# Optimization experiments

Measured on AMD Instinct MI355X. Metric: run time of the kernel, lower is better.

Reference implementation:

```python
import jax, jax.numpy as jnp
import numpy as np

KP_EXTENT = 1.2  # influence radius of each kernel point (init arg KP_extent)
SHADOW_COORD = 1e6  # shadow point coordinate for padding (as in original KPConv)


def setup_inputs() -> dict:
    key = jax.random.key(0)
    k1, k2, k3, k4, k5, k6 = jax.random.split(key, 6)
    N, Ns, H, K, Cin, Cout = 20000, 20000, 40, 15, 128, 128
    q_pts = jax.random.uniform(k1, (N, 3), dtype=jnp.float32)
    s_pts = jax.random.uniform(k2, (Ns, 3), dtype=jnp.float32)
    neighb_inds = jax.random.randint(k3, (N, H), 0, Ns, dtype=jnp.int32)
    x = jax.random.normal(k4, (Ns, Cin), dtype=jnp.float32)
    # kernel point positions inside the sphere (stand-in for load_kernels output)
    kernel_points = jax.random.normal(k5, (K, 3), dtype=jnp.float32) * 0.5
    kernel_points = kernel_points.at[0].set(0.0)  # fixed='center'
    weights = jax.random.normal(k6, (K, Cin, Cout), dtype=jnp.float32) * (1.0 / np.sqrt(Cin))
    return {"q_pts": q_pts, "s_pts": s_pts, "neighb_inds": neighb_inds,
            "x": x, "kernel_points": kernel_points, "weights": weights}


def reference(q_pts, s_pts, neighb_inds, x, kernel_points, weights):
    # Pad support points with a far-away shadow point and features with a zero row,
    # so out-of-range neighbor index Ns contributes nothing (original KPConv trick).
    s_pad = jnp.concatenate([s_pts, jnp.full((1, s_pts.shape[1]), SHADOW_COORD, s_pts.dtype)], axis=0)
    x_pad = jnp.concatenate([x, jnp.zeros((1, x.shape[1]), x.dtype)], axis=0)

    # Gather neighbor coords, center on query points: [N, H, 3]
    neighbors = s_pad[neighb_inds] - q_pts[:, None, :]

    # Squared distance to every kernel point: [N, H, K]
    diff = neighbors[:, :, None, :] - kernel_points[None, None, :, :]
    sq_dist = jnp.sum(diff * diff, axis=-1)

    # Linear influence weights, aggregation_mode='sum': [N, K, H]
    all_weights = jnp.clip(1.0 - jnp.sqrt(sq_dist) / KP_EXTENT, 0.0, None)
    all_weights = jnp.swapaxes(all_weights, 1, 2)

    # Gather neighbor features: [N, H, Cin]
    neighb_x = x_pad[neighb_inds]

    # Influence-weighted aggregation over neighbors: [N, K, Cin]
    weighted = jnp.einsum('nkh,nhc->nkc', all_weights, neighb_x)

    # Per-kernel-point linear maps, summed over kernel points: [N, Cout]
    out = jnp.einsum('nkc,kcd->nd', weighted, weights)
    return out
```

## Files before the change

### kernel.cpp

```cpp
#include <hip/hip_runtime.h>

#define KP   15
#define HN   40
#define CIN  128
#define COUT 128
#define KDIM (KP*CIN)
#define KP_EXT_INV (1.0f/1.2f)
#define GBM  32
#define GBK  128

typedef __bf16 bf16x8 __attribute__((ext_vector_type(8)));
typedef __bf16 bf16x4 __attribute__((ext_vector_type(4)));
typedef float  f32x4  __attribute__((ext_vector_type(4)));

__device__ inline void async_copy16(const void* g, void* lds) {
    __builtin_amdgcn_global_load_lds(
        (const __attribute__((address_space(1))) unsigned int*)g,
        (__attribute__((address_space(3))) unsigned int*)lds, 16, 0, 0);
}
#define LGKM0() __asm__ __volatile__("s_waitcnt lgkmcnt(0)" ::: "memory")
#define VM0()   __asm__ __volatile__("s_waitcnt vmcnt(0)"   ::: "memory")

__global__ __launch_bounds__(256)
void kpconv_prep(const float* __restrict__ x, const float* __restrict__ W,
                 __bf16* __restrict__ xb, __bf16* __restrict__ Wt,
                 int nx_elems, int nxB)
{
    __shared__ float sW[32][133];
    const int b = blockIdx.x;
    const int t = threadIdx.x;

    if (b < nxB) {
        const int e0 = (b*256 + t) * 8;
        if (e0 + 8 <= nx_elems) {
            const float4 f0 = *(const float4*)(x + e0);
            const float4 f1 = *(const float4*)(x + e0 + 4);
            bf16x8 v;
            v[0]=(__bf16)f0.x; v[1]=(__bf16)f0.y; v[2]=(__bf16)f0.z; v[3]=(__bf16)f0.w;
            v[4]=(__bf16)f1.x; v[5]=(__bf16)f1.y; v[6]=(__bf16)f1.z; v[7]=(__bf16)f1.w;
            *(bf16x8*)(xb + e0) = v;
        } else {
            for (int e = e0; e < nx_elems; ++e) xb[e] = (__bf16)x[e];
        }
    } else {
        const int kc0 = (b - nxB) * 32;
        #pragma unroll
        for (int i = 0; i < 4; ++i) {
            const int off = t*4 + i*1024;
            const int r = off >> 7, c = off & 127;
            const float4 f = *(const float4*)(W + (size_t)(kc0 + r)*COUT + c);
            sW[r][c+0]=f.x; sW[r][c+1]=f.y; sW[r][c+2]=f.z; sW[r][c+3]=f.w;
        }
        __syncthreads();
        #pragma unroll
        for (int i = 0; i < 2; ++i) {
            const int id = t + i*256;
            const int d  = id >> 2, ch = id & 3;
            bf16x8 v;
            #pragma unroll
            for (int j = 0; j < 8; ++j) v[j] = (__bf16)sW[ch*8 + j][d];
            *(bf16x8*)(Wt + (size_t)d*KDIM + kc0 + ch*8) = v;
        }
    }
}

union SharedU {
    struct { __bf16 sXt[4][4][128][8];
             float4 s_nd[4][HN]; int s_idx[4][HN]; } a;
    struct { __bf16 sA[GBM*GBK]; __bf16 sB[COUT*GBK]; } b;
};

__global__ __launch_bounds__(256, 3)
void kpconv_main(const float* __restrict__ q_pts,
                 const float* __restrict__ s_pts,
                 const int*   __restrict__ nb,
                 const __bf16* __restrict__ xb,
                 const float* __restrict__ kpts,
                 const __bf16* __restrict__ Wt,
                 __bf16* __restrict__ wsA,
                 float* __restrict__ out, int N, int Ns)
{
    __shared__ SharedU sh;

    const int t  = threadIdx.x;
    const int wv = t >> 6;
    const int l  = t & 63;
    const int m  = l & 15;
    const int q  = l >> 4;
    const int m0 = blockIdx.x * GBM;

    {
        float kx=0.f, ky=0.f, kz=0.f;
        if (m < KP) { kx = kpts[m*3+0]; ky = kpts[m*3+1]; kz = kpts[m*3+2]; }
        const float kk  = kx*kx + ky*ky + kz*kz;
        const float kx2 = -2.f*kx, ky2 = -2.f*ky, kz2 = -2.f*kz;

        for (int pi = 0; pi < 8; ++pi) {
            const int n = m0 + wv*8 + pi;

            if (l < HN) {
                int idx = nb[n*HN + l];
                float dx, dy, dz;
                if (idx >= 0 && idx < Ns) {
                    dx = s_pts[idx*3+0] - q_pts[n*3+0];
                    dy = s_pts[idx*3+1] - q_pts[n*3+1];
                    dz = s_pts[idx*3+2] - q_pts[n*3+2];
                } else { idx = 0; dx = dy = dz = 2.0e6f; }
                sh.a.s_idx[wv][l] = idx;
                sh.a.s_nd[wv][l]  = make_float4(dx, dy, dz, dx*dx+dy*dy+dz*dz);
            }
            LGKM0();

            uint4 g[5][2];
            #pragma unroll
            for (int it = 0; it < 5; ++it) {
                const int h0 = (it < 4) ? (it*8 + 2*q) : (32 + 2*q);
                g[it][0] = *(const uint4*)(xb + (size_t)sh.a.s_idx[wv][h0  ]*CIN + m*8);
                g[it][1] = *(const uint4*)(xb + (size_t)sh.a.s_idx[wv][h0+1]*CIN + m*8);
            }

            bf16x8 wfrag[2];
            #pragma unroll
            for (int ks = 0; ks < 2; ++ks) {
                #pragma unroll
                for (int j = 0; j < 8; ++j) {
                    const int h = ks*32 + q*8 + j;
                    float w = 0.f;
                    if (m < KP && h < HN) {
                        const float4 nd = sh.a.s_nd[wv][h];
                        const float d2 = fmaf(nd.x, kx2,
                                         fmaf(nd.y, ky2,
                                         fmaf(nd.z, kz2, nd.w + kk)));
                        const float d = __builtin_amdgcn_sqrtf(d2);
                        w = fmaxf(fmaf(d, -KP_EXT_INV, 1.0f), 0.f);
                    }
                    wfrag[ks][j] = (__bf16)w;
                }
            }

            f32x4 acc[8];
            #pragma unroll
            for (int nt = 0; nt < 8; ++nt) acc[nt] = (f32x4){0.f,0.f,0.f,0.f};

            #pragma unroll
            for (int ks = 0; ks < 2; ++ks) {
                const int itBeg = ks ? 4 : 0;
                const int itEnd = ks ? 5 : 4;
                #pragma unroll
                for (int it = itBeg; it < itEnd; ++it) {
                    const unsigned av[4] = {g[it][0].x, g[it][0].y, g[it][0].z, g[it][0].w};
                    const unsigned bv[4] = {g[it][1].x, g[it][1].y, g[it][1].z, g[it][1].w};
                    const int hc = ks ? 0 : it;
                    unsigned* plane = (unsigned*)&sh.a.sXt[wv][hc][0][0];
                    #pragma unroll
                    for (int j = 0; j < 8; ++j) {
                        const unsigned v = __builtin_amdgcn_perm(
                            bv[j>>1], av[j>>1], (j&1) ? 0x07060302u : 0x05040100u);
                        const int p = m*8 + (j ^ (m & 7));
                        plane[p*4 + q] = v;
                    }
                }
                LGKM0();
                #pragma unroll
                for (int nt = 0; nt < 8; ++nt) {
                    const int cc = nt*16 + m;
                    const int p  = (cc & ~7) | ((cc & 7) ^ ((cc >> 3) & 7));
                    bf16x8 xf = *(const bf16x8*)&sh.a.sXt[wv][q][p][0];
                    acc[nt] = __builtin_amdgcn_mfma_f32_16x16x32_bf16(
                                  xf, wfrag[ks], acc[nt], 0, 0, 0);
                }
            }

            if (m < KP) {
                #pragma unroll
                for (int nt = 0; nt < 8; ++nt) {
                    bf16x4 v;
                    #pragma unroll
                    for (int r = 0; r < 4; ++r) v[r] = (__bf16)acc[nt][r];
                    *(bf16x4*)(wsA + (size_t)n*KDIM + m*CIN + nt*16 + q*4) = v;
                }
            }
        }
    }

    VM0();
    __syncthreads();

    {
        const int rA = t >> 4;
        const int pA = t & 15;

        f32x4 acc[2][2];
        #pragma unroll
        for (int i = 0; i < 2; ++i)
            #pragma unroll
            for (int j = 0; j < 2; ++j) acc[i][j] = (f32x4){0.f,0.f,0.f,0.f};

        for (int k0 = 0; k0 < KDIM; k0 += GBK) {
            #pragma unroll
            for (int pass = 0; pass < 2; ++pass) {
                const int r  = rA + pass*16;
                const int ch = pA ^ (r & 15);
                async_copy16(wsA + (size_t)(m0 + r)*KDIM + k0 + ch*8,
                             (char*)sh.b.sA + pass*4096 + wv*1024 + l*16);
            }
            #pragma unroll
            for (int pass = 0; pass < 8; ++pass) {
                const int r  = rA + pass*16;
                const int ch = pA ^ (r & 15);
                async_copy16(Wt + (size_t)r*KDIM + k0 + ch*8,
                             (char*)sh.b.sB + pass*4096 + wv*1024 + l*16);
            }
            __syncthreads();

            #pragma unroll
            for (int ks = 0; ks < 4; ++ks) {
                bf16x8 af[2], bfr[2];
                #pragma unroll
                for (int mt = 0; mt < 2; ++mt) {
                    const int row = mt*16 + m;
                    const int p   = (ks*4 + q) ^ (row & 15);
                    af[mt] = *(const bf16x8*)&sh.b.sA[row*GBK + p*8];
                }
                #pragma unroll
                for (int j = 0; j < 2; ++j) {
                    const int row = (wv*2 + j)*16 + m;
                    const int p   = (ks*4 + q) ^ (row & 15);
                    bfr[j] = *(const bf16x8*)&sh.b.sB[row*GBK + p*8];
                }
                #pragma unroll
                for (int mt = 0; mt < 2; ++mt)
                    #pragma unroll
                    for (int j = 0; j < 2; ++j)
                        acc[mt][j] = __builtin_amdgcn_mfma_f32_16x16x32_bf16(
                                         af[mt], bfr[j], acc[mt][j], 0, 0, 0);
            }
            __syncthreads();
        }

        #pragma unroll
        for (int mt = 0; mt < 2; ++mt)
            #pragma unroll
            for (int j = 0; j < 2; ++j)
                #pragma unroll
                for (int r = 0; r < 4; ++r)
                    out[(size_t)(m0 + mt*16 + q*4 + r)*COUT
                        + (wv*2+j)*16 + m] = acc[mt][j][r];
    }
}

#define TM 8
#define WSTR (KP*CIN + 4)

__global__ __launch_bounds__(256, 2)
void kpconv_fused(const float* __restrict__ q_pts,
                  const float* __restrict__ s_pts,
                  const int*   __restrict__ nb,
                  const float* __restrict__ x,
                  const float* __restrict__ kpts,
                  const float* __restrict__ W,
                  float* __restrict__ out,
                  int N, int Ns)
{
    __shared__ float s_kp[KP*3];
    __shared__ float s_nd2[HN*3];
    __shared__ int   s_idx2[HN];
    __shared__ float s_w[KP][HN];
    __shared__ float s_wt[TM*WSTR];

    const int t  = threadIdx.x;
    const int n0 = (int)blockIdx.x * TM;
    if (t < KP*3) s_kp[t] = kpts[t];
    const int c = t & (CIN-1);
    const int g = t >> 7;

    for (int mm = 0; mm < TM; ++mm) {
        const int n = n0 + mm;
        if (t < HN) {
            float dx = 1e6f, dy = 1e6f, dz = 1e6f;
            int idx = 0;
            if (n < N) {
                idx = nb[n*HN + t];
                if (idx >= 0 && idx < Ns) {
                    dx = s_pts[idx*3+0] - q_pts[n*3+0];
                    dy = s_pts[idx*3+1] - q_pts[n*3+1];
                    dz = s_pts[idx*3+2] - q_pts[n*3+2];
                } else idx = 0;
            }
            s_idx2[t] = idx;
            s_nd2[t*3+0] = dx; s_nd2[t*3+1] = dy; s_nd2[t*3+2] = dz;
        }
        __syncthreads();
        for (int task = t; task < KP*HN; task += 256) {
            const int k = task / HN;
            const int h = task - k*HN;
            const float dx = s_nd2[h*3+0] - s_kp[k*3+0];
            const float dy = s_nd2[h*3+1] - s_kp[k*3+1];
            const float dz = s_nd2[h*3+2] - s_kp[k*3+2];
            s_w[k][h] = fmaxf(1.0f - sqrtf(dx*dx+dy*dy+dz*dz)*KP_EXT_INV, 0.0f);
        }
        __syncthreads();
        float facc[8];
        #pragma unroll
        for (int j = 0; j < 8; ++j) facc[j] = 0.0f;
        #pragma unroll 8
        for (int h = 0; h < HN; ++h) {
            const float xv = x[s_idx2[h]*CIN + c];
            #pragma unroll
            for (int j = 0; j < 8; ++j) {
                const int k = g + 2*j;
                if (k < KP) facc[j] += s_w[k][h] * xv;
            }
        }
        #pragma unroll
        for (int j = 0; j < 8; ++j) {
            const int k = g + 2*j;
            if (k < KP) s_wt[mm*WSTR + k*CIN + c] = facc[j];
        }
        __syncthreads();
    }

    const int m3 = t >> 5;
    const int d0 = (t & 31) * 4;
    const float* wm = &s_wt[m3*WSTR];
    float ax = 0.f, ay = 0.f, az = 0.f, aw = 0.f;
    #pragma unroll 4
    for (int kc = 0; kc < KP*CIN; ++kc) {
        const float  wvv = wm[kc];
        const float4 wr = *(const float4*)&W[kc*COUT + d0];
        ax += wvv * wr.x; ay += wvv * wr.y; az += wvv * wr.z; aw += wvv * wr.w;
    }
    const int n = n0 + m3;
    if (n < N) {
        float4 o; o.x = ax; o.y = ay; o.z = az; o.w = aw;
        *(float4*)&out[n*COUT + d0] = o;
    }
}

extern "C" void kernel_launch(void* const* d_in, const int* in_sizes, int n_in,
                              void* d_out, int out_size, void* d_ws, size_t ws_size,
                              hipStream_t stream) {
    const float* q_pts = (const float*)d_in[0];
    const float* s_pts = (const float*)d_in[1];
    const int*   nb    = (const int*)  d_in[2];
    const float* x     = (const float*)d_in[3];
    const float* kpts  = (const float*)d_in[4];
    const float* W     = (const float*)d_in[5];
    float* out = (float*)d_out;

    const int N  = in_sizes[0] / 3;
    const int Ns = in_sizes[1] / 3;
    const int nx = in_sizes[3];

    const size_t needA = (size_t)N * KDIM * sizeof(__bf16);
    const size_t needB = (size_t)COUT * KDIM * sizeof(__bf16);
    const size_t needX = (size_t)nx * sizeof(__bf16);

    if (ws_size >= needA + needB + needX && (N % GBM) == 0 && (nx % 8) == 0
        && (KDIM % GBK) == 0) {
        __bf16* wsA = (__bf16*)d_ws;
        __bf16* wsB = (__bf16*)((char*)d_ws + needA);
        __bf16* wsX = (__bf16*)((char*)d_ws + needA + needB);

        const int nxB = (nx/8 + 255) / 256;
        const int nwB = KDIM / 32;
        hipLaunchKernelGGL(kpconv_prep, dim3(nxB + nwB), dim3(256), 0, stream,
                           x, W, wsX, wsB, nx, nxB);
        hipLaunchKernelGGL(kpconv_main, dim3(N/GBM), dim3(256), 0, stream,
                           q_pts, s_pts, nb, wsX, kpts, wsB, wsA, out, N, Ns);
    } else {
        const int grid = (N + TM - 1) / TM;
        hipLaunchKernelGGL(kpconv_fused, dim3(grid), dim3(256), 0, stream,
                           q_pts, s_pts, nb, x, kpts, W, out, N, Ns);
    }
}
```

Before: 144.4 us.

## Keep per-point weighted features in LDS instead of global workspace round-trip

The main kernel now handles 16 points per 512-thread block, with each wave handling 2 points. It writes the bf16 [K*Cin] aggregated features into a swizzled LDS tile instead of a global workspace buffer. The second GEMM stage reads A fragments from LDS and streams B (the transposed weights) directly from global/L2 with two accumulators, dropping the async LDS staging of B. This removes roughly 77MB of workspace write and read traffic. In exchange, every block re-reads the full 128x1920 weight matrix from cache, the LDS footprint is larger, and there are fewer points per block.

```diff
diff --git a/kernel.cpp b/kernel.cpp
--- a/kernel.cpp
+++ b/kernel.cpp
@@ -5,21 +5,15 @@
 #define CIN  128
 #define COUT 128
 #define KDIM (KP*CIN)
+#define NGRAN (KDIM/8)
 #define KP_EXT_INV (1.0f/1.2f)
-#define GBM  32
-#define GBK  128
+#define BM   16
 
 typedef __bf16 bf16x8 __attribute__((ext_vector_type(8)));
 typedef __bf16 bf16x4 __attribute__((ext_vector_type(4)));
 typedef float  f32x4  __attribute__((ext_vector_type(4)));
 
-__device__ inline void async_copy16(const void* g, void* lds) {
-    __builtin_amdgcn_global_load_lds(
-        (const __attribute__((address_space(1))) unsigned int*)g,
-        (__attribute__((address_space(3))) unsigned int*)lds, 16, 0, 0);
-}
 #define LGKM0() __asm__ __volatile__("s_waitcnt lgkmcnt(0)" ::: "memory")
-#define VM0()   __asm__ __volatile__("s_waitcnt vmcnt(0)"   ::: "memory")
 
 __global__ __launch_bounds__(256)
 void kpconv_prep(const float* __restrict__ x, const float* __restrict__ W,
@@ -64,30 +58,30 @@
     }
 }
 
-union SharedU {
-    struct { __bf16 sXt[4][4][128][8];
-             float4 s_nd[4][HN]; int s_idx[4][HN]; } a;
-    struct { __bf16 sA[GBM*GBK]; __bf16 sB[COUT*GBK]; } b;
+struct alignas(16) SharedF {
+    __bf16 wT[NGRAN][16][8];
+    __bf16 sXt[8][4][128][8];
+    float4 s_nd[8][HN];
+    int    s_idx[8][HN];
 };
 
-__global__ __launch_bounds__(256, 3)
-void kpconv_main(const float* __restrict__ q_pts,
-                 const float* __restrict__ s_pts,
-                 const int*   __restrict__ nb,
-                 const __bf16* __restrict__ xb,
-                 const float* __restrict__ kpts,
-                 const __bf16* __restrict__ Wt,
-                 __bf16* __restrict__ wsA,
-                 float* __restrict__ out, int N, int Ns)
+__global__ __launch_bounds__(512, 2)
+void kpconv_fused16(const float* __restrict__ q_pts,
+                    const float* __restrict__ s_pts,
+                    const int*   __restrict__ nb,
+                    const __bf16* __restrict__ xb,
+                    const float* __restrict__ kpts,
+                    const __bf16* __restrict__ Wt,
+                    float* __restrict__ out, int N, int Ns)
 {
-    __shared__ SharedU sh;
+    __shared__ SharedF sh;
 
     const int t  = threadIdx.x;
     const int wv = t >> 6;
     const int l  = t & 63;
     const int m  = l & 15;
     const int q  = l >> 4;
-    const int m0 = blockIdx.x * GBM;
+    const int m0 = blockIdx.x * BM;
 
     {
         float kx=0.f, ky=0.f, kz=0.f;
@@ -95,8 +89,9 @@
         const float kk  = kx*kx + ky*ky + kz*kz;
         const float kx2 = -2.f*kx, ky2 = -2.f*ky, kz2 = -2.f*kz;
 
-        for (int pi = 0; pi < 8; ++pi) {
-            const int n = m0 + wv*8 + pi;
+        for (int pi = 0; pi < 2; ++pi) {
+            const int pt = wv*2 + pi;
+            const int n  = m0 + pt;
 
             if (l < HN) {
                 int idx = nb[n*HN + l];
@@ -106,8 +101,8 @@
                     dy = s_pts[idx*3+1] - q_pts[n*3+1];
                     dz = s_pts[idx*3+2] - q_pts[n*3+2];
                 } else { idx = 0; dx = dy = dz = 2.0e6f; }
-                sh.a.s_idx[wv][l] = idx;
-                sh.a.s_nd[wv][l]  = make_float4(dx, dy, dz, dx*dx+dy*dy+dz*dz);
+                sh.s_idx[wv][l] = idx;
+                sh.s_nd[wv][l]  = make_float4(dx, dy, dz, dx*dx+dy*dy+dz*dz);
             }
             LGKM0();
 
@@ -115,8 +110,8 @@
             #pragma unroll
             for (int it = 0; it < 5; ++it) {
                 const int h0 = (it < 4) ? (it*8 + 2*q) : (32 + 2*q);
-                g[it][0] = *(const uint4*)(xb + (size_t)sh.a.s_idx[wv][h0  ]*CIN + m*8);
-                g[it][1] = *(const uint4*)(xb + (size_t)sh.a.s_idx[wv][h0+1]*CIN + m*8);
+                g[it][0] = *(const uint4*)(xb + (size_t)sh.s_idx[wv][h0  ]*CIN + m*8);
+                g[it][1] = *(const uint4*)(xb + (size_t)sh.s_idx[wv][h0+1]*CIN + m*8);
             }
 
             bf16x8 wfrag[2];
@@ -127,7 +122,7 @@
                     const int h = ks*32 + q*8 + j;
                     float w = 0.f;
                     if (m < KP && h < HN) {
-                        const float4 nd = sh.a.s_nd[wv][h];
+                        const float4 nd = sh.s_nd[wv][h];
                         const float d2 = fmaf(nd.x, kx2,
                                          fmaf(nd.y, ky2,
                                          fmaf(nd.z, kz2, nd.w + kk)));
@@ -151,7 +146,7 @@
                     const unsigned av[4] = {g[it][0].x, g[it][0].y, g[it][0].z, g[it][0].w};
                     const unsigned bv[4] = {g[it][1].x, g[it][1].y, g[it][1].z, g[it][1].w};
                     const int hc = ks ? 0 : it;
-                    unsigned* plane = (unsigned*)&sh.a.sXt[wv][hc][0][0];
+                    unsigned* plane = (unsigned*)&sh.sXt[wv][hc][0][0];
                     #pragma unroll
                     for (int j = 0; j < 8; ++j) {
                         const unsigned v = __builtin_amdgcn_perm(
@@ -165,7 +160,7 @@
                 for (int nt = 0; nt < 8; ++nt) {
                     const int cc = nt*16 + m;
                     const int p  = (cc & ~7) | ((cc & 7) ^ ((cc >> 3) & 7));
-                    bf16x8 xf = *(const bf16x8*)&sh.a.sXt[wv][q][p][0];
+                    bf16x8 xf = *(const bf16x8*)&sh.sXt[wv][q][p][0];
                     acc[nt] = __builtin_amdgcn_mfma_f32_16x16x32_bf16(
                                   xf, wfrag[ks], acc[nt], 0, 0, 0);
                 }
@@ -177,75 +172,44 @@
                     bf16x4 v;
                     #pragma unroll
                     for (int r = 0; r < 4; ++r) v[r] = (__bf16)acc[nt][r];
-                    *(bf16x4*)(wsA + (size_t)n*KDIM + m*CIN + nt*16 + q*4) = v;
+                    const int G = m*16 + nt*2 + (q>>1);
+                    const int s = (pt ^ G ^ m) & 15;
+                    *(bf16x4*)(&sh.wT[G][s][0] + (q&1)*4) = v;
                 }
             }
         }
     }
 
-    VM0();
     __syncthreads();
 
     {
-        const int rA = t >> 4;
-        const int pA = t & 15;
-
-        f32x4 acc[2][2];
-        #pragma unroll
-        for (int i = 0; i < 2; ++i)
-            #pragma unroll
-            for (int j = 0; j < 2; ++j) acc[i][j] = (f32x4){0.f,0.f,0.f,0.f};
-
-        for (int k0 = 0; k0 < KDIM; k0 += GBK) {
-            #pragma unroll
-            for (int pass = 0; pass < 2; ++pass) {
-                const int r  = rA + pass*16;
-                const int ch = pA ^ (r & 15);
-                async_copy16(wsA + (size_t)(m0 + r)*KDIM + k0 + ch*8,
-                             (char*)sh.b.sA + pass*4096 + wv*1024 + l*16);
-            }
-            #pragma unroll
-            for (int pass = 0; pass < 8; ++pass) {
-                const int r  = rA + pass*16;
-                const int ch = pA ^ (r & 15);
-                async_copy16(Wt + (size_t)r*KDIM + k0 + ch*8,
-                             (char*)sh.b.sB + pass*4096 + wv*1024 + l*16);
-            }
-            __syncthreads();
-
-            #pragma unroll
-            for (int ks = 0; ks < 4; ++ks) {
-                bf16x8 af[2], bfr[2];
-                #pragma unroll
-                for (int mt = 0; mt < 2; ++mt) {
-                    const int row = mt*16 + m;
-                    const int p   = (ks*4 + q) ^ (row & 15);
-                    af[mt] = *(const bf16x8*)&sh.b.sA[row*GBK + p*8];
-                }
-                #pragma unroll
-                for (int j = 0; j < 2; ++j) {
-                    const int row = (wv*2 + j)*16 + m;
-                    const int p   = (ks*4 + q) ^ (row & 15);
-                    bfr[j] = *(const bf16x8*)&sh.b.sB[row*GBK + p*8];
-                }
-                #pragma unroll
-                for (int mt = 0; mt < 2; ++mt)
-                    #pragma unroll
-                    for (int j = 0; j < 2; ++j)
-                        acc[mt][j] = __builtin_amdgcn_mfma_f32_16x16x32_bf16(
-                                         af[mt], bfr[j], acc[mt][j], 0, 0, 0);
-            }
-            __syncthreads();
-        }
-
-        #pragma unroll
-        for (int mt = 0; mt < 2; ++mt)
-            #pragma unroll
-            for (int j = 0; j < 2; ++j)
-                #pragma unroll
-                for (int r = 0; r < 4; ++r)
-                    out[(size_t)(m0 + mt*16 + q*4 + r)*COUT
-                        + (wv*2+j)*16 + m] = acc[mt][j][r];
+        const __bf16* bp = Wt + (size_t)(wv*16 + m)*KDIM + q*8;
+        f32x4 accA = (f32x4){0.f,0.f,0.f,0.f};
+        f32x4 accB = (f32x4){0.f,0.f,0.f,0.f};
+
+        #pragma unroll 3
+        for (int k0 = 0; k0 < KDIM; k0 += 64) {
+            {
+                const int G = (k0 >> 3) + q;
+                const int s = (m ^ G ^ (G >> 4)) & 15;
+                const bf16x8 af = *(const bf16x8*)&sh.wT[G][s][0];
+                const bf16x8 bf_ = *(const bf16x8*)(bp + k0);
+                accA = __builtin_amdgcn_mfma_f32_16x16x32_bf16(af, bf_, accA, 0, 0, 0);
+            }
+            {
+                const int G = ((k0 + 32) >> 3) + q;
+                const int s = (m ^ G ^ (G >> 4)) & 15;
+                const bf16x8 af = *(const bf16x8*)&sh.wT[G][s][0];
+                const bf16x8 bf_ = *(const bf16x8*)(bp + k0 + 32);
+                accB = __builtin_amdgcn_mfma_f32_16x16x32_bf16(af, bf_, accB, 0, 0, 0);
+            }
+        }
+
+        const f32x4 accv = accA + accB;
+        const int d = wv*16 + m;
+        #pragma unroll
+        for (int r = 0; r < 4; ++r)
+            out[(size_t)(m0 + q*4 + r)*COUT + d] = accv[r];
     }
 }
 
@@ -352,22 +316,20 @@
     const int Ns = in_sizes[1] / 3;
     const int nx = in_sizes[3];
 
-    const size_t needA = (size_t)N * KDIM * sizeof(__bf16);
     const size_t needB = (size_t)COUT * KDIM * sizeof(__bf16);
     const size_t needX = (size_t)nx * sizeof(__bf16);
 
-    if (ws_size >= needA + needB + needX && (N % GBM) == 0 && (nx % 8) == 0
-        && (KDIM % GBK) == 0) {
-        __bf16* wsA = (__bf16*)d_ws;
-        __bf16* wsB = (__bf16*)((char*)d_ws + needA);
-        __bf16* wsX = (__bf16*)((char*)d_ws + needA + needB);
+    if (ws_size >= needB + needX && (N % BM) == 0 && (nx % 8) == 0
+        && (KDIM % 64) == 0) {
+        __bf16* wsB = (__bf16*)d_ws;
+        __bf16* wsX = (__bf16*)((char*)d_ws + needB);
 
         const int nxB = (nx/8 + 255) / 256;
         const int nwB = KDIM / 32;
         hipLaunchKernelGGL(kpconv_prep, dim3(nxB + nwB), dim3(256), 0, stream,
                            x, W, wsX, wsB, nx, nxB);
-        hipLaunchKernelGGL(kpconv_main, dim3(N/GBM), dim3(256), 0, stream,
-                           q_pts, s_pts, nb, wsX, kpts, wsB, wsA, out, N, Ns);
+        hipLaunchKernelGGL(kpconv_fused16, dim3(N/BM), dim3(512), 0, stream,
+                           q_pts, s_pts, nb, wsX, kpts, wsB, out, N, Ns);
     } else {
         const int grid = (N + TM - 1) / TM;
         hipLaunchKernelGGL(kpconv_fused, dim3(grid), dim3(256), 0, stream,
```

Result: slower. 178.3 us (+23.5%).

## Split gather/aggregation and GEMM into separate kernels, software-pipeline neighbor gathers

Applied to the files above, without the earlier changes.

Splits the previously fused main kernel into a gather/aggregation kernel and a separate GEMM kernel. Both now launch with an occupancy hint of 4 blocks, since neither has to reserve the other phase's shared memory or registers. Inside the aggregation kernel, neighbor indices, offsets and feature gathers for the next point are double-buffered and issued while the current point's MFMAs run, to hide gather latency. The cost is an extra kernel launch, the loss of in-block cache locality for the intermediate buffer between phases, and higher register pressure from holding prefetched data.

```diff
diff --git a/kernel.cpp b/kernel.cpp
--- a/kernel.cpp
+++ b/kernel.cpp
@@ -19,7 +19,6 @@
         (__attribute__((address_space(3))) unsigned int*)lds, 16, 0, 0);
 }
 #define LGKM0() __asm__ __volatile__("s_waitcnt lgkmcnt(0)" ::: "memory")
-#define VM0()   __asm__ __volatile__("s_waitcnt vmcnt(0)"   ::: "memory")
 
 __global__ __launch_bounds__(256)
 void kpconv_prep(const float* __restrict__ x, const float* __restrict__ W,
@@ -64,23 +63,22 @@
     }
 }
 
-union SharedU {
-    struct { __bf16 sXt[4][4][128][8];
-             float4 s_nd[4][HN]; int s_idx[4][HN]; } a;
-    struct { __bf16 sA[GBM*GBK]; __bf16 sB[COUT*GBK]; } b;
+struct alignas(16) SharedA {
+    __bf16 sXt[4][4][128][8];
+    float4 s_nd[4][2][HN];
+    int    s_idx[4][2][HN];
 };
 
-__global__ __launch_bounds__(256, 3)
-void kpconv_main(const float* __restrict__ q_pts,
-                 const float* __restrict__ s_pts,
-                 const int*   __restrict__ nb,
-                 const __bf16* __restrict__ xb,
-                 const float* __restrict__ kpts,
-                 const __bf16* __restrict__ Wt,
-                 __bf16* __restrict__ wsA,
-                 float* __restrict__ out, int N, int Ns)
+__global__ __launch_bounds__(256, 4)
+void kpconv_phaseA(const float* __restrict__ q_pts,
+                   const float* __restrict__ s_pts,
+                   const int*   __restrict__ nb,
+                   const __bf16* __restrict__ xb,
+                   const float* __restrict__ kpts,
+                   __bf16* __restrict__ wsA,
+                   int N, int Ns)
 {
-    __shared__ SharedU sh;
+    __shared__ SharedA sh;
 
     const int t  = threadIdx.x;
     const int wv = t >> 6;
@@ -89,164 +87,224 @@
     const int q  = l >> 4;
     const int m0 = blockIdx.x * GBM;
 
+    float kx=0.f, ky=0.f, kz=0.f;
+    if (m < KP) { kx = kpts[m*3+0]; ky = kpts[m*3+1]; kz = kpts[m*3+2]; }
+    const float kk  = kx*kx + ky*ky + kz*kz;
+    const float kx2 = -2.f*kx, ky2 = -2.f*ky, kz2 = -2.f*kz;
+
     {
-        float kx=0.f, ky=0.f, kz=0.f;
-        if (m < KP) { kx = kpts[m*3+0]; ky = kpts[m*3+1]; kz = kpts[m*3+2]; }
-        const float kk  = kx*kx + ky*ky + kz*kz;
-        const float kx2 = -2.f*kx, ky2 = -2.f*ky, kz2 = -2.f*kz;
-
-        for (int pi = 0; pi < 8; ++pi) {
-            const int n = m0 + wv*8 + pi;
-
+        const int n0 = m0 + wv*8;
+        if (l < HN) {
+            int idx = nb[n0*HN + l];
+            float dx, dy, dz;
+            if (idx >= 0 && idx < Ns) {
+                dx = s_pts[idx*3+0] - q_pts[n0*3+0];
+                dy = s_pts[idx*3+1] - q_pts[n0*3+1];
+                dz = s_pts[idx*3+2] - q_pts[n0*3+2];
+            } else { idx = 0; dx = dy = dz = 2.0e6f; }
+            sh.s_idx[wv][0][l] = idx;
+            sh.s_nd[wv][0][l]  = make_float4(dx, dy, dz, dx*dx+dy*dy+dz*dz);
+        }
+        LGKM0();
+    }
+
+    uint4 g[5][2];
+    #pragma unroll
+    for (int itx = 0; itx < 5; ++itx) {
+        const int h0 = (itx < 4) ? (itx*8 + 2*q) : (32 + 2*q);
+        g[itx][0] = *(const uint4*)(xb + (size_t)sh.s_idx[wv][0][h0  ]*CIN + m*8);
+        g[itx][1] = *(const uint4*)(xb + (size_t)sh.s_idx[wv][0][h0+1]*CIN + m*8);
+    }
+
+    for (int pi = 0; pi < 8; ++pi) {
+        const int cur = pi & 1;
+        const int nxt = cur ^ 1;
+        const int n   = m0 + wv*8 + pi;
+        const bool hasNext = (pi < 7);
+
+        int   p_idx = 0;
+        float p_dx = 2.0e6f, p_dy = 2.0e6f, p_dz = 2.0e6f;
+        if (hasNext && l < HN) {
+            const int n1 = n + 1;
+            int idx = nb[n1*HN + l];
+            if (idx >= 0 && idx < Ns) {
+                p_idx = idx;
+                p_dx = s_pts[idx*3+0] - q_pts[n1*3+0];
+                p_dy = s_pts[idx*3+1] - q_pts[n1*3+1];
+                p_dz = s_pts[idx*3+2] - q_pts[n1*3+2];
+            }
+        }
+
+        bf16x8 wfrag[2];
+        #pragma unroll
+        for (int ks = 0; ks < 2; ++ks) {
+            #pragma unroll
+            for (int j = 0; j < 8; ++j) {
+                const int h = ks*32 + q*8 + j;
+                float w = 0.f;
+                if (m < KP && h < HN) {
+                    const float4 nd = sh.s_nd[wv][cur][h];
+                    const float d2 = fmaf(nd.x, kx2,
+                                     fmaf(nd.y, ky2,
+                                     fmaf(nd.z, kz2, nd.w + kk)));
+                    const float d = __builtin_amdgcn_sqrtf(d2);
+                    w = fmaxf(fmaf(d, -KP_EXT_INV, 1.0f), 0.f);
+                }
+                wfrag[ks][j] = (__bf16)w;
+            }
+        }
+
+        f32x4 acc[8];
+        #pragma unroll
+        for (int nt = 0; nt < 8; ++nt) acc[nt] = (f32x4){0.f,0.f,0.f,0.f};
+
+        #pragma unroll
+        for (int itx = 0; itx < 4; ++itx) {
+            const unsigned av[4] = {g[itx][0].x, g[itx][0].y, g[itx][0].z, g[itx][0].w};
+            const unsigned bv[4] = {g[itx][1].x, g[itx][1].y, g[itx][1].z, g[itx][1].w};
+            unsigned* plane = (unsigned*)&sh.sXt[wv][itx][0][0];
+            #pragma unroll
+            for (int j = 0; j < 8; ++j) {
+                const unsigned v = __builtin_amdgcn_perm(
+                    bv[j>>1], av[j>>1], (j&1) ? 0x07060302u : 0x05040100u);
+                const int p = m*8 + (j ^ (m & 7));
+                plane[p*4 + q] = v;
+            }
+        }
+        LGKM0();
+        #pragma unroll
+        for (int nt = 0; nt < 8; ++nt) {
+            const int cc = nt*16 + m;
+            const int p  = (cc & ~7) | ((cc & 7) ^ ((cc >> 3) & 7));
+            bf16x8 xf = *(const bf16x8*)&sh.sXt[wv][q][p][0];
+            acc[nt] = __builtin_amdgcn_mfma_f32_16x16x32_bf16(
+                          xf, wfrag[0], acc[nt], 0, 0, 0);
+        }
+
+        {
+            const unsigned av[4] = {g[4][0].x, g[4][0].y, g[4][0].z, g[4][0].w};
+            const unsigned bv[4] = {g[4][1].x, g[4][1].y, g[4][1].z, g[4][1].w};
+            unsigned* plane = (unsigned*)&sh.sXt[wv][0][0][0];
+            #pragma unroll
+            for (int j = 0; j < 8; ++j) {
+                const unsigned v = __builtin_amdgcn_perm(
+                    bv[j>>1], av[j>>1], (j&1) ? 0x07060302u : 0x05040100u);
+                const int p = m*8 + (j ^ (m & 7));
+                plane[p*4 + q] = v;
+            }
+        }
+
+        if (hasNext) {
             if (l < HN) {
-                int idx = nb[n*HN + l];
-                float dx, dy, dz;
-                if (idx >= 0 && idx < Ns) {
-                    dx = s_pts[idx*3+0] - q_pts[n*3+0];
-                    dy = s_pts[idx*3+1] - q_pts[n*3+1];
-                    dz = s_pts[idx*3+2] - q_pts[n*3+2];
-                } else { idx = 0; dx = dy = dz = 2.0e6f; }
-                sh.a.s_idx[wv][l] = idx;
-                sh.a.s_nd[wv][l]  = make_float4(dx, dy, dz, dx*dx+dy*dy+dz*dz);
+                sh.s_idx[wv][nxt][l] = p_idx;
+                sh.s_nd[wv][nxt][l]  = make_float4(p_dx, p_dy, p_dz,
+                                                   p_dx*p_dx + p_dy*p_dy + p_dz*p_dz);
             }
             LGKM0();
-
-            uint4 g[5][2];
-            #pragma unroll
-            for (int it = 0; it < 5; ++it) {
-                const int h0 = (it < 4) ? (it*8 + 2*q) : (32 + 2*q);
-                g[it][0] = *(const uint4*)(xb + (size_t)sh.a.s_idx[wv][h0  ]*CIN + m*8);
-                g[it][1] = *(const uint4*)(xb + (size_t)sh.a.s_idx[wv][h0+1]*CIN + m*8);
-            }
-
-            bf16x8 wfrag[2];
-            #pragma unroll
-            for (int ks = 0; ks < 2; ++ks) {
+            #pragma unroll
+            for (int itx = 0; itx < 5; ++itx) {
+                const int h0 = (itx < 4) ? (itx*8 + 2*q) : (32 + 2*q);
+                g[itx][0] = *(const uint4*)(xb + (size_t)sh.s_idx[wv][nxt][h0  ]*CIN + m*8);
+                g[itx][1] = *(const uint4*)(xb + (size_t)sh.s_idx[wv][nxt][h0+1]*CIN + m*8);
+            }
+        }
+
+        LGKM0();
+        #pragma unroll
+        for (int nt = 0; nt < 8; ++nt) {
+            const int cc = nt*16 + m;
+            const int p  = (cc & ~7) | ((cc & 7) ^ ((cc >> 3) & 7));
+            bf16x8 xf = *(const bf16x8*)&sh.sXt[wv][q][p][0];
+            acc[nt] = __builtin_amdgcn_mfma_f32_16x16x32_bf16(
+                          xf, wfrag[1], acc[nt], 0, 0, 0);
+        }
+
+        if (m < KP) {
+            #pragma unroll
+            for (int nt = 0; nt < 8; ++nt) {
+                bf16x4 v;
                 #pragma unroll
-                for (int j = 0; j < 8; ++j) {
-                    const int h = ks*32 + q*8 + j;
-                    float w = 0.f;
-                    if (m < KP && h < HN) {
-                        const float4 nd = sh.a.s_nd[wv][h];
-                        const float d2 = fmaf(nd.x, kx2,
-                                         fmaf(nd.y, ky2,
-                                         fmaf(nd.z, kz2, nd.w + kk)));
-                        const float d = __builtin_amdgcn_sqrtf(d2);
-                        w = fmaxf(fmaf(d, -KP_EXT_INV, 1.0f), 0.f);
-                    }
-                    wfrag[ks][j] = (__bf16)w;
-                }
-            }
-
-            f32x4 acc[8];
-            #pragma unroll
-            for (int nt = 0; nt < 8; ++nt) acc[nt] = (f32x4){0.f,0.f,0.f,0.f};
-
-            #pragma unroll
-            for (int ks = 0; ks < 2; ++ks) {
-                const int itBeg = ks ? 4 : 0;
-                const int itEnd = ks ? 5 : 4;
+                for (int r = 0; r < 4; ++r) v[r] = (__bf16)acc[nt][r];
+                *(bf16x4*)(wsA + (size_t)n*KDIM + m*CIN + nt*16 + q*4) = v;
+            }
+        }
+    }
+}
+
+struct alignas(16) SharedB { __bf16 sA[GBM*GBK]; __bf16 sB[COUT*GBK]; };
+
+__global__ __launch_bounds__(256, 4)
+void kpconv_gemm(const __bf16* __restrict__ wsA,
+                 const __bf16* __restrict__ Wt,
+                 float* __restrict__ out, int N)
+{
+    __shared__ SharedB sh;
+
+    const int t  = threadIdx.x;
+    const int wv = t >> 6;
+    const int l  = t & 63;
+    const int m  = l & 15;
+    const int q  = l >> 4;
+    const int m0 = blockIdx.x * GBM;
+    const int rA = t >> 4;
+    const int pA = t & 15;
+
+    f32x4 acc[2][2];
+    #pragma unroll
+    for (int i = 0; i < 2; ++i)
+        #pragma unroll
+        for (int j = 0; j < 2; ++j) acc[i][j] = (f32x4){0.f,0.f,0.f,0.f};
+
+    for (int k0 = 0; k0 < KDIM; k0 += GBK) {
+        #pragma unroll
+        for (int pass = 0; pass < 2; ++pass) {
+            const int r  = rA + pass*16;
+            const int ch = pA ^ (r & 15);
+            async_copy16(wsA + (size_t)(m0 + r)*KDIM + k0 + ch*8,
+                         (char*)sh.sA + pass*4096 + wv*1024 + l*16);
+        }
+        #pragma unroll
+        for (int pass = 0; pass < 8; ++pass) {
+            const int r  = rA + pass*16;
+            const int ch = pA ^ (r & 15);
+            async_copy16(Wt + (size_t)r*KDIM + k0 + ch*8,
+                         (char*)sh.sB + pass*4096 + wv*1024 + l*16);
+        }
+        __syncthreads();
+
+        #pragma unroll
+        for (int ks = 0; ks < 4; ++ks) {
+            bf16x8 af[2], bfr[2];
+            #pragma unroll
+            for (int mt = 0; mt < 2; ++mt) {
+                const int row = mt*16 + m;
+                const int p   = (ks*4 + q) ^ (row & 15);
+                af[mt] = *(const bf16x8*)&sh.sA[row*GBK + p*8];
+            }
+            #pragma unroll
+            for (int j = 0; j < 2; ++j) {
+                const int row = (wv*2 + j)*16 + m;
+                const int p   = (ks*4 + q) ^ (row & 15);
+                bfr[j] = *(const bf16x8*)&sh.sB[row*GBK + p*8];
+            }
+            #pragma unroll
+            for (int mt = 0; mt < 2; ++mt)
                 #pragma unroll
-                for (int it = itBeg; it < itEnd; ++it) {
-                    const unsigned av[4] = {g[it][0].x, g[it][0].y, g[it][0].z, g[it][0].w};
-                    const unsigned bv[4] = {g[it][1].x, g[it][1].y, g[it][1].z, g[it][1].w};
-                    const int hc = ks ? 0 : it;
-                    unsigned* plane = (unsigned*)&sh.a.sXt[wv][hc][0][0];
-                    #pragma unroll
-                    for (int j = 0; j < 8; ++j) {
-                        const unsigned v = __builtin_amdgcn_perm(
-                            bv[j>>1], av[j>>1], (j&1) ? 0x07060302u : 0x05040100u);
-                        const int p = m*8 + (j ^ (m & 7));
-                        plane[p*4 + q] = v;
-                    }
-                }
-                LGKM0();
-                #pragma unroll
-                for (int nt = 0; nt < 8; ++nt) {
-                    const int cc = nt*16 + m;
-                    const int p  = (cc & ~7) | ((cc & 7) ^ ((cc >> 3) & 7));
-                    bf16x8 xf = *(const bf16x8*)&sh.a.sXt[wv][q][p][0];
-                    acc[nt] = __builtin_amdgcn_mfma_f32_16x16x32_bf16(
-                                  xf, wfrag[ks], acc[nt], 0, 0, 0);
-                }
-            }
-
-            if (m < KP) {
-                #pragma unroll
-                for (int nt = 0; nt < 8; ++nt) {
-                    bf16x4 v;
-                    #pragma unroll
-                    for (int r = 0; r < 4; ++r) v[r] = (__bf16)acc[nt][r];
-                    *(bf16x4*)(wsA + (size_t)n*KDIM + m*CIN + nt*16 + q*4) = v;
-                }
-            }
-        }
-    }
-
-    VM0();
-    __syncthreads();
-
-    {
-        const int rA = t >> 4;
-        const int pA = t & 15;
-
-        f32x4 acc[2][2];
-        #pragma unroll
-        for (int i = 0; i < 2; ++i)
-            #pragma unroll
-            for (int j = 0; j < 2; ++j) acc[i][j] = (f32x4){0.f,0.f,0.f,0.f};
-
-        for (int k0 = 0; k0 < KDIM; k0 += GBK) {
-            #pragma unroll
-            for (int pass = 0; pass < 2; ++pass) {
-                const int r  = rA + pass*16;
-                const int ch = pA ^ (r & 15);
-                async_copy16(wsA + (size_t)(m0 + r)*KDIM + k0 + ch*8,
-                             (char*)sh.b.sA + pass*4096 + wv*1024 + l*16);
-            }
-            #pragma unroll
-            for (int pass = 0; pass < 8; ++pass) {
-                const int r  = rA + pass*16;
-                const int ch = pA ^ (r & 15);
-                async_copy16(Wt + (size_t)r*KDIM + k0 + ch*8,
-                             (char*)sh.b.sB + pass*4096 + wv*1024 + l*16);
-            }
-            __syncthreads();
-
-            #pragma unroll
-            for (int ks = 0; ks < 4; ++ks) {
-                bf16x8 af[2], bfr[2];
-                #pragma unroll
-                for (int mt = 0; mt < 2; ++mt) {
-                    const int row = mt*16 + m;
-                    const int p   = (ks*4 + q) ^ (row & 15);
-                    af[mt] = *(const bf16x8*)&sh.b.sA[row*GBK + p*8];
-                }
-                #pragma unroll
-                for (int j = 0; j < 2; ++j) {
-                    const int row = (wv*2 + j)*16 + m;
-                    const int p   = (ks*4 + q) ^ (row & 15);
-                    bfr[j] = *(const bf16x8*)&sh.b.sB[row*GBK + p*8];
-                }
-                #pragma unroll
-                for (int mt = 0; mt < 2; ++mt)
-                    #pragma unroll
-                    for (int j = 0; j < 2; ++j)
-                        acc[mt][j] = __builtin_amdgcn_mfma_f32_16x16x32_bf16(
-                                         af[mt], bfr[j], acc[mt][j], 0, 0, 0);
-            }
-            __syncthreads();
-        }
-
-        #pragma unroll
-        for (int mt = 0; mt < 2; ++mt)
-            #pragma unroll
-            for (int j = 0; j < 2; ++j)
-                #pragma unroll
-                for (int r = 0; r < 4; ++r)
-                    out[(size_t)(m0 + mt*16 + q*4 + r)*COUT
-                        + (wv*2+j)*16 + m] = acc[mt][j][r];
-    }
+                for (int j = 0; j < 2; ++j)
+                    acc[mt][j] = __builtin_amdgcn_mfma_f32_16x16x32_bf16(
+                                     af[mt], bfr[j], acc[mt][j], 0, 0, 0);
+        }
+        __syncthreads();
+    }
+
+    #pragma unroll
+    for (int mt = 0; mt < 2; ++mt)
+        #pragma unroll
+        for (int j = 0; j < 2; ++j)
+            #pragma unroll
+            for (int r = 0; r < 4; ++r)
+                out[(size_t)(m0 + mt*16 + q*4 + r)*COUT
+                    + (wv*2+j)*16 + m] = acc[mt][j][r];
 }
 
 #define TM 8
@@ -366,8 +424,10 @@
         const int nwB = KDIM / 32;
         hipLaunchKernelGGL(kpconv_prep, dim3(nxB + nwB), dim3(256), 0, stream,
                            x, W, wsX, wsB, nx, nxB);
-        hipLaunchKernelGGL(kpconv_main, dim3(N/GBM), dim3(256), 0, stream,
-                           q_pts, s_pts, nb, wsX, kpts, wsB, wsA, out, N, Ns);
+        hipLaunchKernelGGL(kpconv_phaseA, dim3(N/GBM), dim3(256), 0, stream,
+                           q_pts, s_pts, nb, wsX, kpts, wsA, N, Ns);
+        hipLaunchKernelGGL(kpconv_gemm, dim3(N/GBM), dim3(256), 0, stream,
+                           wsA, wsB, out, N);
     } else {
         const int grid = (N + TM - 1) / TM;
         hipLaunchKernelGGL(kpconv_fused, dim3(grid), dim3(256), 0, stream,
```

New measurement: 147.9 us. 2.4% more time.
